# Kernel optimization log

Measured on AMD Instinct MI355X. Metric: run time of the kernel, lower is better.

The kernel has to match this reference:

```python
import jax, jax.numpy as jnp
import numpy as np

N_LAYERS = 20
EPS = 1e-7      # GENConv eps added to relu'd messages
BN_EPS = 1e-5   # torch BatchNorm1d default eps
N_NODES, N_EDGES, N_GRAPHS, D, H = 100_000, 400_000, 4096, 128, 256


def _bn(x, g, b):
    # BatchNorm1d in training mode: batch statistics over the node dim
    mu = jnp.mean(x, axis=0)
    var = jnp.var(x, axis=0)
    return (x - mu) * jax.lax.rsqrt(var + BN_EPS) * g + b


def setup_inputs() -> dict:
    key = jax.random.key(0)
    ks = jax.random.split(key, 12)
    L = N_LAYERS
    rn = lambda k, s, sc: jax.random.normal(k, s, dtype=jnp.float32) * sc
    return dict(
        x=jax.random.randint(ks[0], (N_NODES, 9), 0, 2, dtype=jnp.int32),
        edge_index=jax.random.randint(ks[1], (2, N_EDGES), 0, N_NODES, dtype=jnp.int32),
        edge_attr=jax.random.randint(ks[2], (N_EDGES, 3), 0, 2, dtype=jnp.int32),
        batch=jnp.sort(jax.random.randint(ks[3], (N_NODES,), 0, N_GRAPHS, dtype=jnp.int32)),
        # AtomEncoder: 9 tables (max size 119), padded into one array
        atom_emb=rn(ks[4], (9, 119, D), 0.1),
        # per-layer BondEncoder: 3 tables (sizes 5,6,2) padded to 6
        bond_emb=rn(ks[5], (L, 3, 6, D), 0.1),
        W1=rn(ks[6], (L, D, H), 0.05), b1=jnp.zeros((L, H), jnp.float32),
        g1=jnp.ones((L, H), jnp.float32), be1=jnp.zeros((L, H), jnp.float32),
        W2=rn(ks[7], (L, H, H), 0.05), b2=jnp.zeros((L, H), jnp.float32),
        g2=jnp.ones((L, H), jnp.float32), be2=jnp.zeros((L, H), jnp.float32),
        W3=rn(ks[8], (L, H, D), 0.05), b3=jnp.zeros((L, D), jnp.float32),
        t=jnp.ones((L,), jnp.float32),
        norm_g=jnp.ones((L, D), jnp.float32), norm_b=jnp.zeros((L, D), jnp.float32),
        predW=rn(ks[9], (D, 1), 0.05), predb=jnp.zeros((1,), jnp.float32),
    )


def _gen_conv(h, src, dst, edge_attr, bond_l, W1, b1, g1, be1, W2, b2, g2, be2, W3, b3, t):
    N = h.shape[0]
    # BondEncoder: sum of 3 embedding lookups
    eemb = bond_l[0][edge_attr[:, 0]] + bond_l[1][edge_attr[:, 1]] + bond_l[2][edge_attr[:, 2]]
    msg = jax.nn.relu(h[src] + eemb) + EPS            # [E, D]
    # scatter_softmax over destination nodes, per channel, temperature t
    scaled = msg * t
    mx = jax.ops.segment_max(scaled, dst, num_segments=N)
    mx = jnp.where(jnp.isfinite(mx), mx, 0.0)         # isolated nodes -> -inf guard
    ex = jnp.exp(scaled - mx[dst])
    denom = jax.ops.segment_sum(ex, dst, num_segments=N)
    w = ex / jnp.maximum(denom[dst], EPS)
    m = jax.ops.segment_sum(msg * w, dst, num_segments=N)
    hh = h + m
    # MLP channels [D, 2D, 2D, D], batch norm + relu on hidden layers, last linear
    a = jax.nn.relu(_bn(hh @ W1 + b1, g1, be1))
    a = jax.nn.relu(_bn(a @ W2 + b2, g2, be2))
    return a @ W3 + b3


def reference(x, edge_index, edge_attr, batch, atom_emb, bond_emb, W1, b1, g1, be1,
              W2, b2, g2, be2, W3, b3, t, norm_g, norm_b, predW, predb):
    N = x.shape[0]
    src, dst = edge_index[0], edge_index[1]
    # AtomEncoder: sum of 9 embedding lookups
    h = atom_emb[0][x[:, 0]]
    for i in range(1, 9):
        h = h + atom_emb[i][x[:, i]]
    lp = lambda l: (bond_emb[l], W1[l], b1[l], g1[l], be1[l], W2[l], b2[l],
                    g2[l], be2[l], W3[l], b3[l], t[l])
    # res+ block (dropout omitted: eval mode)
    h = _gen_conv(h, src, dst, edge_attr, *lp(0))
    for l in range(1, N_LAYERS):
        h2 = jax.nn.relu(_bn(h, norm_g[l - 1], norm_b[l - 1]))
        h = _gen_conv(h2, src, dst, edge_attr, *lp(l)) + h
    h = _bn(h, norm_g[N_LAYERS - 1], norm_b[N_LAYERS - 1])
    # global mean pool over graphs
    cnt = jax.ops.segment_sum(jnp.ones((N, 1), jnp.float32), batch, num_segments=N_GRAPHS)
    hg = jax.ops.segment_sum(h, batch, num_segments=N_GRAPHS) / jnp.maximum(cnt, 1.0)
    return hg @ predW + predb                          # [N_GRAPHS, 1]
```

## Files before the change

kernel.cpp:

```cpp
#include <hip/hip_runtime.h>
#include <math.h>

#define GEPS 1e-7f
#define BNEPS 1e-5f
#define NCOPY 32
#define CSTR 1536

typedef unsigned short u16;
typedef unsigned int   u32;

typedef _Float16 f16x8 __attribute__((ext_vector_type(8)));
typedef float    f32x4 __attribute__((ext_vector_type(4)));

__device__ __forceinline__ float h2f(u16 u){
  _Float16 x = __builtin_bit_cast(_Float16, u); return (float)x;
}
__device__ __forceinline__ u16 f2h(float f){
  _Float16 x = (_Float16)f; return __builtin_bit_cast(u16, x);
}

typedef __attribute__((address_space(1))) const void* as1p;
typedef __attribute__((address_space(3))) void*       as3p;
__device__ __forceinline__ void dma16(const u16* g, _Float16* l){
  __builtin_amdgcn_global_load_lds((as1p)g, (as3p)l, 16, 0, 0);
}

__global__ __launch_bounds__(256) void k_zero_i(int* __restrict__ p, int n){
  int i = blockIdx.x*256 + threadIdx.x;
  if (i < n) p[i] = 0;
}
__global__ __launch_bounds__(256) void k_zero_f(float* __restrict__ p, int n){
  int i = blockIdx.x*256 + threadIdx.x;
  if (i < n) p[i] = 0.f;
}

__global__ __launch_bounds__(256) void k_hist(const int* __restrict__ dst, int E,
                                              int* __restrict__ cnt){
  int e = blockIdx.x*256 + threadIdx.x;
  if (e < E) atomicAdd(&cnt[dst[e]], 1);
}

__global__ __launch_bounds__(256) void k_blocksum(const int* __restrict__ cnt, int N,
                                                  int* __restrict__ part){
  __shared__ int s[256];
  int t = threadIdx.x, i = blockIdx.x*256 + t;
  s[t] = (i < N) ? cnt[i] : 0;
  __syncthreads();
  for (int off = 128; off > 0; off >>= 1){
    if (t < off) s[t] += s[t + off];
    __syncthreads();
  }
  if (t == 0) part[blockIdx.x] = s[0];
}

__global__ __launch_bounds__(1024) void k_scanpart(int* __restrict__ part, int NB){
  __shared__ int s[1024];
  int t = threadIdx.x;
  int v = (t < NB) ? part[t] : 0;
  s[t] = v;
  __syncthreads();
  for (int off = 1; off < 1024; off <<= 1){
    int u = (t >= off) ? s[t-off] : 0;
    __syncthreads();
    s[t] += u;
    __syncthreads();
  }
  if (t < NB) part[t] = s[t] - v;
}

__global__ __launch_bounds__(256) void k_scanapply(const int* __restrict__ cnt,
    const int* __restrict__ part, int N, int E,
    int* __restrict__ offs, int* __restrict__ cursor){
  __shared__ int s[256];
  int t = threadIdx.x, i = blockIdx.x*256 + t;
  int v = (i < N) ? cnt[i] : 0;
  s[t] = v;
  __syncthreads();
  for (int off = 1; off < 256; off <<= 1){
    int u = (t >= off) ? s[t-off] : 0;
    __syncthreads();
    s[t] += u;
    __syncthreads();
  }
  int ex = part[blockIdx.x] + s[t] - v;
  if (i < N){
    offs[i]   = ex;
    cursor[i] = ex;
    if (i == N-1) offs[N] = ex + v;
  }
}

__global__ __launch_bounds__(256) void k_scatter(const int* __restrict__ src,
    const int* __restrict__ dst, const int* __restrict__ attr, int E,
    int* __restrict__ cursor, int* __restrict__ esort){
  int e = blockIdx.x*256 + threadIdx.x;
  if (e >= E) return;
  int d = dst[e];
  int pos = atomicAdd(&cursor[d], 1);
  int a = (src[e] & 0x1ffff)
        | ((attr[3*(size_t)e]   & 15) << 17)
        | ((attr[3*(size_t)e+1] & 15) << 21)
        | ((attr[3*(size_t)e+2] & 15) << 25);
  esort[pos] = a;
}

__global__ __launch_bounds__(256) void k_wtrans(const float* __restrict__ W,
    u16* __restrict__ Wt, int K, int Nout, int total){
  int id = blockIdx.x*256 + threadIdx.x;
  if (id >= total) return;
  int k   = id % K;
  int rem = id / K;
  int n   = rem % Nout;
  int l   = rem / Nout;
  Wt[id] = f2h(W[((size_t)l*K + k)*Nout + n]);
}

__global__ __launch_bounds__(256) void k_atom(const int* __restrict__ x,
    const float* __restrict__ emb, float* __restrict__ h, u16* __restrict__ h16, int N){
  int d = threadIdx.x & 127;
  int n = (blockIdx.x << 1) + (threadIdx.x >> 7);
  if (n >= N) return;
  float s = 0.f;
  #pragma unroll
  for (int i = 0; i < 9; ++i){
    int idx = x[(size_t)n*9 + i];
    s += emb[((size_t)i*119 + idx)*128 + d];
  }
  h[(size_t)n*128 + d]   = s;
  h16[(size_t)n*128 + d] = f2h(s);
}

__global__ __launch_bounds__(256) void k_redstats(const float* __restrict__ Cl,
                                                  float* __restrict__ out){
  int t = threadIdx.x;
  float s = 0.f;
  #pragma unroll
  for (int c = 0; c < NCOPY; ++c) s += Cl[c*CSTR + 1024 + t];
  out[t] = s;
}

template<bool PRE_BN>
__global__ __launch_bounds__(256)
void k_edge(const u16* __restrict__ h16,
    const int* __restrict__ offs, const int* __restrict__ esort,
    const float* __restrict__ bond,
    const float* __restrict__ tptr,
    const float* __restrict__ ssum_, const float* __restrict__ ssq_,
    const float* __restrict__ g, const float* __restrict__ b,
    u16* __restrict__ hh, int N, float invN){
  __shared__ float sg[128], sv[128];
  int tid = threadIdx.x;
  if (PRE_BN){
    if (tid < 128){
      float mu  = ssum_[tid]*invN;
      float var = fmaxf(ssq_[tid]*invN - mu*mu, 0.f);
      float rs  = rsqrtf(var + BNEPS);
      float s   = g[tid]*rs;
      sg[tid] = s;
      sv[tid] = b[tid] - mu*s;
    }
    __syncthreads();
  }
  int lane = tid & 63;
  int n = (blockIdx.x << 2) + (tid >> 6);
  if (n >= N) return;
  int c0 = lane << 1;
  float tl = *tptr;
  float sg0=1.f, sv0=0.f, sg1=1.f, sv1=0.f;
  if (PRE_BN){ sg0=sg[c0]; sv0=sv[c0]; sg1=sg[c0+1]; sv1=sv[c0+1]; }

  int s0 = offs[n], s1 = offs[n+1];
  float den0 = 0.f, acc0 = 0.f, den1 = 0.f, acc1 = 0.f;
  if (s0 < s1){
    int se = esort[s0];
    int sidx = se & 0x1ffff;
    u32 hv = *(const u32*)(h16 + (size_t)sidx*128 + c0);
    float2 e0 = *(const float2*)(bond + ((se>>17)&15)*128 + c0);
    float2 e1 = *(const float2*)(bond + (6 + ((se>>21)&15))*128 + c0);
    float2 e2 = *(const float2*)(bond + (12 + ((se>>25)&15))*128 + c0);
    for (int e = s0; e < s1; ++e){
      u32 hvN = hv; float2 e0N = e0, e1N = e1, e2N = e2;
      if (e + 1 < s1){
        int seN = esort[e+1];
        int sidxN = seN & 0x1ffff;
        hvN = *(const u32*)(h16 + (size_t)sidxN*128 + c0);
        e0N = *(const float2*)(bond + ((seN>>17)&15)*128 + c0);
        e1N = *(const float2*)(bond + (6 + ((seN>>21)&15))*128 + c0);
        e2N = *(const float2*)(bond + (12 + ((seN>>25)&15))*128 + c0);
      }
      float x0 = h2f((u16)(hv & 0xffff));
      float x1 = h2f((u16)(hv >> 16));
      if (PRE_BN){
        x0 = fmaxf(x0*sg0 + sv0, 0.f);
        x1 = fmaxf(x1*sg1 + sv1, 0.f);
      }
      float m0 = fmaxf(x0 + e0.x + e1.x + e2.x, 0.f) + GEPS;
      float m1 = fmaxf(x1 + e0.y + e1.y + e2.y, 0.f) + GEPS;
      float p0 = __expf(m0*tl);
      float p1 = __expf(m1*tl);
      den0 += p0; acc0 += p0*m0;
      den1 += p1; acc1 += p1*m1;
      hv = hvN; e0 = e0N; e1 = e1N; e2 = e2N;
    }
  }
  u32 hv = *(const u32*)(h16 + (size_t)n*128 + c0);
  float x0 = h2f((u16)(hv & 0xffff));
  float x1 = h2f((u16)(hv >> 16));
  if (PRE_BN){
    x0 = fmaxf(x0*sg0 + sv0, 0.f);
    x1 = fmaxf(x1*sg1 + sv1, 0.f);
  }
  float r0 = x0 + acc0 / fmaxf(den0, GEPS);
  float r1 = x1 + acc1 / fmaxf(den1, GEPS);
  u32 pk = (u32)f2h(r0) | ((u32)f2h(r1) << 16);
  *((u32*)hh + (size_t)n*64 + lane) = pk;
}

template<bool TRANSFORM, bool OUT32>
__global__ __launch_bounds__(256)
void k_gemm(const u16* __restrict__ A, int lda,
            const u16* __restrict__ Wt,
            const float* __restrict__ bias,
            const float* __restrict__ sIn, const float* __restrict__ qIn,
            const float* __restrict__ gam, const float* __restrict__ bet,
            const float* __restrict__ resid,
            void* __restrict__ outv, int ldo,
            u16* __restrict__ out16,
            float* __restrict__ sOut, float* __restrict__ qOut,
            int M, int K){
  __shared__ __align__(16) _Float16 As[2][4096];
  __shared__ __align__(16) _Float16 Bs[2][4096];
  __shared__ float sc[256], shv[256];
  __shared__ float redS[256], redQ[256];

  int tid = threadIdx.x;
  int lane = tid & 63;
  int w    = tid >> 6;
  int wm = w & 1, wn = w >> 1;
  int quad = lane >> 4, ln = lane & 15;
  int mBase = blockIdx.x * 128;
  int cBase = blockIdx.y * 128;

  int dc0 = tid, dc1 = 256 + tid;
  int f0 = dc0 >> 6, l20 = dc0 & 63;
  int f1 = dc1 >> 6, l21 = dc1 & 63;
  int kA0 = (l20 >> 4) << 3, kA1 = (l21 >> 4) << 3;
  int rA0 = mBase + f0*16 + (l20 & 15); if (rA0 >= M) rA0 = M - 1;
  int rA1 = mBase + f1*16 + (l21 & 15); if (rA1 >= M) rA1 = M - 1;
  const u16* apA0 = A + (size_t)rA0*lda + kA0;
  const u16* apA1 = A + (size_t)rA1*lda + kA1;
  const u16* bp0  = Wt + (size_t)(cBase + f0*16 + (l20 & 15))*K + kA0;
  const u16* bp1  = Wt + (size_t)(cBase + f1*16 + (l21 & 15))*K + kA1;

  dma16(apA0, &As[0][dc0*8]);
  dma16(apA1, &As[0][dc1*8]);
  dma16(bp0,  &Bs[0][dc0*8]);
  dma16(bp1,  &Bs[0][dc1*8]);

  if (TRANSFORM){
    float inv = 1.f/(float)M;
    for (int k = tid; k < K; k += 256){
      float s_ = 0.f, q_ = 0.f;
      #pragma unroll
      for (int c = 0; c < NCOPY; ++c){ s_ += sIn[c*CSTR + k]; q_ += qIn[c*CSTR + k]; }
      float mu  = s_*inv;
      float var = fmaxf(q_*inv - mu*mu, 0.f);
      float rs  = rsqrtf(var + BNEPS);
      float sg  = gam[k]*rs;
      sc[k]  = sg;
      shv[k] = bet[k] - mu*sg;
    }
  }

  f32x4 acc[4][4];
  #pragma unroll
  for (int i = 0; i < 4; ++i)
    #pragma unroll
    for (int j = 0; j < 4; ++j)
      acc[i][j] = (f32x4){0.f,0.f,0.f,0.f};

  int kTiles = K >> 5;
  for (int kt = 0; kt < kTiles; ++kt){
    __syncthreads();
    int cb = kt & 1, nbuf = cb ^ 1;
    if (kt + 1 < kTiles){
      int k1 = (kt + 1) << 5;
      dma16(apA0 + k1, &As[nbuf][dc0*8]);
      dma16(apA1 + k1, &As[nbuf][dc1*8]);
      dma16(bp0 + k1,  &Bs[nbuf][dc0*8]);
      dma16(bp1 + k1,  &Bs[nbuf][dc1*8]);
    }
    f16x8 af[4], bf[4];
    #pragma unroll
    for (int i = 0; i < 4; ++i)
      af[i] = *(const f16x8*)(&As[cb][(4*wm + i)*512 + lane*8]);
    if (TRANSFORM){
      int kb = kt*32 + quad*8;
      f32x4 s0 = *(const f32x4*)(&sc[kb]);
      f32x4 s1 = *(const f32x4*)(&sc[kb+4]);
      f32x4 v0 = *(const f32x4*)(&shv[kb]);
      f32x4 v1 = *(const f32x4*)(&shv[kb+4]);
      #pragma unroll
      for (int i = 0; i < 4; ++i){
        f16x8 a = af[i], o;
        o[0] = (_Float16)fmaxf((float)a[0]*s0[0] + v0[0], 0.f);
        o[1] = (_Float16)fmaxf((float)a[1]*s0[1] + v0[1], 0.f);
        o[2] = (_Float16)fmaxf((float)a[2]*s0[2] + v0[2], 0.f);
        o[3] = (_Float16)fmaxf((float)a[3]*s0[3] + v0[3], 0.f);
        o[4] = (_Float16)fmaxf((float)a[4]*s1[0] + v1[0], 0.f);
        o[5] = (_Float16)fmaxf((float)a[5]*s1[1] + v1[1], 0.f);
        o[6] = (_Float16)fmaxf((float)a[6]*s1[2] + v1[2], 0.f);
        o[7] = (_Float16)fmaxf((float)a[7]*s1[3] + v1[3], 0.f);
        af[i] = o;
      }
    }
    #pragma unroll
    for (int j = 0; j < 4; ++j)
      bf[j] = *(const f16x8*)(&Bs[cb][(4*wn + j)*512 + lane*8]);
    #pragma unroll
    for (int i = 0; i < 4; ++i)
      #pragma unroll
      for (int j = 0; j < 4; ++j)
        acc[i][j] = __builtin_amdgcn_mfma_f32_16x16x32_f16(af[i], bf[j], acc[i][j], 0, 0, 0);
  }

  float bv[4];
  #pragma unroll
  for (int j = 0; j < 4; ++j) bv[j] = bias[cBase + 64*wn + 16*j + ln];
  float ps[4] = {0,0,0,0}, pq[4] = {0,0,0,0};

  #pragma unroll
  for (int i = 0; i < 4; ++i){
    int rbase = mBase + 64*wm + 16*i + quad*4;
    #pragma unroll
    for (int r = 0; r < 4; ++r){
      int row = rbase + r;
      if (row < M){
        #pragma unroll
        for (int j = 0; j < 4; ++j){
          int col = cBase + 64*wn + 16*j + ln;
          size_t off = (size_t)row*ldo + col;
          float v = acc[i][j][r] + bv[j];
          if (OUT32){
            float* out = (float*)outv;
            if (resid) v += resid[off];
            out[off] = v;
            if (out16) out16[off] = f2h(v);
            ps[j] += v; pq[j] += v*v;
          } else {
            u16* out = (u16*)outv;
            u16 q = f2h(v);
            out[off] = q;
            float vr = h2f(q);
            ps[j] += vr; pq[j] += vr*vr;
          }
        }
      }
    }
  }
  #pragma unroll
  for (int j = 0; j < 4; ++j){
    float s = ps[j], q = pq[j];
    s += __shfl_xor(s, 16, 64);  q += __shfl_xor(q, 16, 64);
    s += __shfl_xor(s, 32, 64);  q += __shfl_xor(q, 32, 64);
    if (quad == 0){
      int col = 64*wn + 16*j + ln;
      redS[wm*128 + col] = s;
      redQ[wm*128 + col] = q;
    }
  }
  __syncthreads();
  if (tid < 128){
    float s = redS[tid] + redS[128 + tid];
    float q = redQ[tid] + redQ[128 + tid];
    int cof = (blockIdx.x & (NCOPY-1))*CSTR + cBase + tid;
    atomicAdd(&sOut[cof], s);
    atomicAdd(&qOut[cof], q);
  }
}

__global__ __launch_bounds__(256) void k_pool(const float* __restrict__ h,
    const float* __restrict__ ssum, const float* __restrict__ ssq,
    const float* __restrict__ g, const float* __restrict__ b,
    const float* __restrict__ predW, const int* __restrict__ batch,
    float* __restrict__ pool, float* __restrict__ cnt, int N){
  int lane = threadIdx.x & 63;
  int n = (blockIdx.x << 2) + (threadIdx.x >> 6);
  if (n >= N) return;
  float inv = 1.f / (float)N;
  float v = 0.f;
  #pragma unroll
  for (int d = lane; d < 128; d += 64){
    float mu  = ssum[d]*inv;
    float var = fmaxf(ssq[d]*inv - mu*mu, 0.f);
    float rs  = rsqrtf(var + BNEPS);
    float bn  = (h[(size_t)n*128 + d] - mu)*(g[d]*rs) + b[d];
    v += bn * predW[d];
  }
  #pragma unroll
  for (int off = 32; off > 0; off >>= 1) v += __shfl_down(v, off, 64);
  if (lane == 0){
    int gi = batch[n];
    atomicAdd(&pool[gi], v);
    atomicAdd(&cnt[gi], 1.f);
  }
}

__global__ __launch_bounds__(256) void k_final(const float* __restrict__ pool,
    const float* __restrict__ cnt, const float* __restrict__ predb,
    float* __restrict__ out, int G){
  int g = blockIdx.x*256 + threadIdx.x;
  if (g < G) out[g] = pool[g] / fmaxf(cnt[g], 1.f) + predb[0];
}

extern "C" void kernel_launch(void* const* d_in, const int* in_sizes, int n_in,
                              void* d_out, int out_size, void* d_ws, size_t ws_size,
                              hipStream_t stream){
  const int*   x        = (const int*)d_in[0];
  const int*   eidx     = (const int*)d_in[1];
  const int*   eattr    = (const int*)d_in[2];
  const int*   batch    = (const int*)d_in[3];
  const float* atom_emb = (const float*)d_in[4];
  const float* bond_emb = (const float*)d_in[5];
  const float* W1 = (const float*)d_in[6];
  const float* b1 = (const float*)d_in[7];
  const float* g1 = (const float*)d_in[8];
  const float* be1= (const float*)d_in[9];
  const float* W2 = (const float*)d_in[10];
  const float* b2 = (const float*)d_in[11];
  const float* g2 = (const float*)d_in[12];
  const float* be2= (const float*)d_in[13];
  const float* W3 = (const float*)d_in[14];
  const float* b3 = (const float*)d_in[15];
  const float* tt = (const float*)d_in[16];
  const float* ng = (const float*)d_in[17];
  const float* nb = (const float*)d_in[18];
  const float* predW = (const float*)d_in[19];
  const float* predb = (const float*)d_in[20];
  float* out = (float*)d_out;

  const int N = in_sizes[3];
  const int E = in_sizes[1] / 2;
  const int L = in_sizes[16];
  const int G = out_size;
  const int D = 128, H = 256;
  const float invN = 1.f / (float)N;

  char* ws = (char*)d_ws;
  size_t off = 0;
  auto carve = [&](size_t bytes)->void*{
    void* p = ws + off;
    off += (bytes + 511) & ~(size_t)511;
    return p;
  };
  float* h   = (float*)carve((size_t)N*D*4);
  u16*   y1  = (u16*)  carve((size_t)N*H*2);
  u16*   y2  = (u16*)  carve((size_t)N*H*2);
  u16*   hh  = y2;
  u16*   h16 = y1;
  u16*   Wt1 = (u16*) carve((size_t)L*H*D*2);
  u16*   Wt2 = (u16*) carve((size_t)L*H*H*2);
  u16*   Wt3 = (u16*) carve((size_t)L*D*H*2);
  int*  offs   = (int*)carve((size_t)(N+1)*4);
  int*  cursor = (int*)carve((size_t)N*4);
  int*  cnt    = (int*)carve((size_t)N*4);
  int*  part   = (int*)carve(1024*4);
  int*  esort  = (int*)carve((size_t)E*4);
  float* stats = (float*)carve((size_t)L*NCOPY*CSTR*4);
  float* fstat = (float*)carve((size_t)L*256*4);
  float* pool = (float*)carve((size_t)G*4);
  float* cntg = (float*)carve((size_t)G*4);

  int NB = (N + 255) / 256;

  k_zero_i   <<<NB, 256, 0, stream>>>(cnt, N);
  k_hist     <<<(E+255)/256, 256, 0, stream>>>(eidx + E, E, cnt);
  k_blocksum <<<NB, 256, 0, stream>>>(cnt, N, part);
  k_scanpart <<<1, 1024, 0, stream>>>(part, NB);
  k_scanapply<<<NB, 256, 0, stream>>>(cnt, part, N, E, offs, cursor);
  k_scatter  <<<(E+255)/256, 256, 0, stream>>>(eidx, eidx + E, eattr, E, cursor, esort);
  k_atom     <<<(N+1)/2, 256, 0, stream>>>(x, atom_emb, h, h16, N);
  k_zero_f   <<<(L*NCOPY*CSTR+255)/256, 256, 0, stream>>>(stats, L*NCOPY*CSTR);

  k_wtrans<<<((L*H*D)+255)/256, 256, 0, stream>>>(W1, Wt1, D, H, L*H*D);
  k_wtrans<<<((L*H*H)+255)/256, 256, 0, stream>>>(W2, Wt2, H, H, L*H*H);
  k_wtrans<<<((L*D*H)+255)/256, 256, 0, stream>>>(W3, Wt3, H, D, L*D*H);

  int mb = (N + 127) / 128;
  int eb = (N + 3) / 4;
  for (int l = 0; l < L; ++l){
    float* Cl = stats + (size_t)l*NCOPY*CSTR;
    const float* bondl = bond_emb + (size_t)l*3*6*D;
    if (l == 0){
      k_edge<false><<<eb, 256, 0, stream>>>(h16, offs, esort, bondl, tt + l,
          nullptr, nullptr, nullptr, nullptr, hh, N, invN);
    } else {
      float* fs = fstat + (size_t)(l-1)*256;
      k_edge<true><<<eb, 256, 0, stream>>>(h16, offs, esort, bondl, tt + l,
          fs, fs + 128, ng + (size_t)(l-1)*D, nb + (size_t)(l-1)*D,
          hh, N, invN);
    }
    k_gemm<false,false><<<dim3(mb,2), 256, 0, stream>>>(hh, D,
        Wt1 + (size_t)l*H*D, b1 + (size_t)l*H,
        nullptr, nullptr, nullptr, nullptr, nullptr,
        y1, H, nullptr, Cl + 0, Cl + 256, N, D);
    k_gemm<true,false><<<dim3(mb,2), 256, 0, stream>>>(y1, H,
        Wt2 + (size_t)l*H*H, b2 + (size_t)l*H,
        Cl + 0, Cl + 256, g1 + (size_t)l*H, be1 + (size_t)l*H, nullptr,
        y2, H, nullptr, Cl + 512, Cl + 768, N, H);
    k_gemm<true,true><<<dim3(mb,1), 256, 0, stream>>>(y2, H,
        Wt3 + (size_t)l*D*H, b3 + (size_t)l*D,
        Cl + 512, Cl + 768, g2 + (size_t)l*H, be2 + (size_t)l*H,
        (l ? h : nullptr),
        h, D, h16, Cl + 1024, Cl + 1152, N, H);
    k_redstats<<<1, 256, 0, stream>>>(Cl, fstat + (size_t)l*256);
  }

  float* fsL = fstat + (size_t)(L-1)*256;
  k_zero_f<<<(G+255)/256, 256, 0, stream>>>(pool, G);
  k_zero_f<<<(G+255)/256, 256, 0, stream>>>(cntg, G);
  k_pool  <<<(N+3)/4, 256, 0, stream>>>(h, fsL, fsL + 128,
      ng + (size_t)(L-1)*D, nb + (size_t)(L-1)*D, predW, batch, pool, cntg, N);
  k_final <<<(G+255)/256, 256, 0, stream>>>(pool, cntg, predb, out, G);
}
```

Baseline: 4.860 ms.

## Precombine bond embeddings and shrink GEMM M-tile to 64 rows

Precomputes, per layer, all 72 combinations of the three bond embedding tables, so the edge kernel does one float2 lookup per edge instead of three loads and two adds. Separately, the GEMM block tile shrinks from 128 to 64 rows, with each of the four waves covering all 64 rows and 32 columns. This doubles the grid and removes the LDS cross-wave stats reduction and its barrier, at the cost of more global atomics on the stats copies and less reuse of the B tile per block.

```diff
diff --git a/kernel.cpp b/kernel.cpp
--- a/kernel.cpp
+++ b/kernel.cpp
@@ -97,11 +97,20 @@
   if (e >= E) return;
   int d = dst[e];
   int pos = atomicAdd(&cursor[d], 1);
-  int a = (src[e] & 0x1ffff)
-        | ((attr[3*(size_t)e]   & 15) << 17)
-        | ((attr[3*(size_t)e+1] & 15) << 21)
-        | ((attr[3*(size_t)e+2] & 15) << 25);
-  esort[pos] = a;
+  int comb = attr[3*(size_t)e]*12 + attr[3*(size_t)e+1]*2 + attr[3*(size_t)e+2];
+  esort[pos] = (src[e] & 0x1ffff) | (comb << 17);
+}
+
+__global__ __launch_bounds__(256) void k_comb(const float* __restrict__ bond_emb,
+    float* __restrict__ comb, int total){
+  int id = blockIdx.x*256 + threadIdx.x;
+  if (id >= total) return;
+  int d = id & 127;
+  int c = (id >> 7) % 72;
+  int l = (id >> 7) / 72;
+  int a0 = c/12, a1 = (c/2)%6, a2 = c&1;
+  const float* b = bond_emb + (size_t)l*3*6*128;
+  comb[id] = b[a0*128 + d] + b[(6 + a1)*128 + d] + b[(12 + a2)*128 + d];
 }
 
 __global__ __launch_bounds__(256) void k_wtrans(const float* __restrict__ W,
@@ -143,7 +152,7 @@
 __global__ __launch_bounds__(256)
 void k_edge(const u16* __restrict__ h16,
     const int* __restrict__ offs, const int* __restrict__ esort,
-    const float* __restrict__ bond,
+    const float* __restrict__ comb,
     const float* __restrict__ tptr,
     const float* __restrict__ ssum_, const float* __restrict__ ssq_,
     const float* __restrict__ g, const float* __restrict__ b,
@@ -173,20 +182,14 @@
   float den0 = 0.f, acc0 = 0.f, den1 = 0.f, acc1 = 0.f;
   if (s0 < s1){
     int se = esort[s0];
-    int sidx = se & 0x1ffff;
-    u32 hv = *(const u32*)(h16 + (size_t)sidx*128 + c0);
-    float2 e0 = *(const float2*)(bond + ((se>>17)&15)*128 + c0);
-    float2 e1 = *(const float2*)(bond + (6 + ((se>>21)&15))*128 + c0);
-    float2 e2 = *(const float2*)(bond + (12 + ((se>>25)&15))*128 + c0);
+    u32 hv = *(const u32*)(h16 + (size_t)(se & 0x1ffff)*128 + c0);
+    float2 ev = *(const float2*)(comb + (se >> 17)*128 + c0);
     for (int e = s0; e < s1; ++e){
-      u32 hvN = hv; float2 e0N = e0, e1N = e1, e2N = e2;
+      u32 hvN = hv; float2 evN = ev;
       if (e + 1 < s1){
         int seN = esort[e+1];
-        int sidxN = seN & 0x1ffff;
-        hvN = *(const u32*)(h16 + (size_t)sidxN*128 + c0);
-        e0N = *(const float2*)(bond + ((seN>>17)&15)*128 + c0);
-        e1N = *(const float2*)(bond + (6 + ((seN>>21)&15))*128 + c0);
-        e2N = *(const float2*)(bond + (12 + ((seN>>25)&15))*128 + c0);
+        hvN = *(const u32*)(h16 + (size_t)(seN & 0x1ffff)*128 + c0);
+        evN = *(const float2*)(comb + (seN >> 17)*128 + c0);
       }
       float x0 = h2f((u16)(hv & 0xffff));
       float x1 = h2f((u16)(hv >> 16));
@@ -194,13 +197,13 @@
         x0 = fmaxf(x0*sg0 + sv0, 0.f);
         x1 = fmaxf(x1*sg1 + sv1, 0.f);
       }
-      float m0 = fmaxf(x0 + e0.x + e1.x + e2.x, 0.f) + GEPS;
-      float m1 = fmaxf(x1 + e0.y + e1.y + e2.y, 0.f) + GEPS;
+      float m0 = fmaxf(x0 + ev.x, 0.f) + GEPS;
+      float m1 = fmaxf(x1 + ev.y, 0.f) + GEPS;
       float p0 = __expf(m0*tl);
       float p1 = __expf(m1*tl);
       den0 += p0; acc0 += p0*m0;
       den1 += p1; acc1 += p1*m1;
-      hv = hvN; e0 = e0N; e1 = e1N; e2 = e2N;
+      hv = hvN; ev = evN;
     }
   }
   u32 hv = *(const u32*)(h16 + (size_t)n*128 + c0);
@@ -228,34 +231,31 @@
             u16* __restrict__ out16,
             float* __restrict__ sOut, float* __restrict__ qOut,
             int M, int K){
-  __shared__ __align__(16) _Float16 As[2][4096];
+  __shared__ __align__(16) _Float16 As[2][2048];
   __shared__ __align__(16) _Float16 Bs[2][4096];
   __shared__ float sc[256], shv[256];
-  __shared__ float redS[256], redQ[256];
 
   int tid = threadIdx.x;
   int lane = tid & 63;
-  int w    = tid >> 6;
-  int wm = w & 1, wn = w >> 1;
+  int wn   = tid >> 6;
   int quad = lane >> 4, ln = lane & 15;
-  int mBase = blockIdx.x * 128;
+  int mBase = blockIdx.x * 64;
   int cBase = blockIdx.y * 128;
 
+  int fA = tid >> 6, lA = tid & 63;
+  int kA = (lA >> 4) << 3;
+  int rA = mBase + fA*16 + (lA & 15); if (rA >= M) rA = M - 1;
+  const u16* apA = A + (size_t)rA*lda + kA;
   int dc0 = tid, dc1 = 256 + tid;
   int f0 = dc0 >> 6, l20 = dc0 & 63;
   int f1 = dc1 >> 6, l21 = dc1 & 63;
-  int kA0 = (l20 >> 4) << 3, kA1 = (l21 >> 4) << 3;
-  int rA0 = mBase + f0*16 + (l20 & 15); if (rA0 >= M) rA0 = M - 1;
-  int rA1 = mBase + f1*16 + (l21 & 15); if (rA1 >= M) rA1 = M - 1;
-  const u16* apA0 = A + (size_t)rA0*lda + kA0;
-  const u16* apA1 = A + (size_t)rA1*lda + kA1;
-  const u16* bp0  = Wt + (size_t)(cBase + f0*16 + (l20 & 15))*K + kA0;
-  const u16* bp1  = Wt + (size_t)(cBase + f1*16 + (l21 & 15))*K + kA1;
-
-  dma16(apA0, &As[0][dc0*8]);
-  dma16(apA1, &As[0][dc1*8]);
-  dma16(bp0,  &Bs[0][dc0*8]);
-  dma16(bp1,  &Bs[0][dc1*8]);
+  int kB0 = (l20 >> 4) << 3, kB1 = (l21 >> 4) << 3;
+  const u16* bp0 = Wt + (size_t)(cBase + f0*16 + (l20 & 15))*K + kB0;
+  const u16* bp1 = Wt + (size_t)(cBase + f1*16 + (l21 & 15))*K + kB1;
+
+  dma16(apA, &As[0][dc0*8]);
+  dma16(bp0, &Bs[0][dc0*8]);
+  dma16(bp1, &Bs[0][dc1*8]);
 
   if (TRANSFORM){
     float inv = 1.f/(float)M;
@@ -272,11 +272,11 @@
     }
   }
 
-  f32x4 acc[4][4];
+  f32x4 acc[4][2];
   #pragma unroll
   for (int i = 0; i < 4; ++i)
     #pragma unroll
-    for (int j = 0; j < 4; ++j)
+    for (int j = 0; j < 2; ++j)
       acc[i][j] = (f32x4){0.f,0.f,0.f,0.f};
 
   int kTiles = K >> 5;
@@ -285,15 +285,14 @@
     int cb = kt & 1, nbuf = cb ^ 1;
     if (kt + 1 < kTiles){
       int k1 = (kt + 1) << 5;
-      dma16(apA0 + k1, &As[nbuf][dc0*8]);
-      dma16(apA1 + k1, &As[nbuf][dc1*8]);
-      dma16(bp0 + k1,  &Bs[nbuf][dc0*8]);
-      dma16(bp1 + k1,  &Bs[nbuf][dc1*8]);
-    }
-    f16x8 af[4], bf[4];
+      dma16(apA + k1, &As[nbuf][dc0*8]);
+      dma16(bp0 + k1, &Bs[nbuf][dc0*8]);
+      dma16(bp1 + k1, &Bs[nbuf][dc1*8]);
+    }
+    f16x8 af[4], bf[2];
     #pragma unroll
     for (int i = 0; i < 4; ++i)
-      af[i] = *(const f16x8*)(&As[cb][(4*wm + i)*512 + lane*8]);
+      af[i] = *(const f16x8*)(&As[cb][i*512 + lane*8]);
     if (TRANSFORM){
       int kb = kt*32 + quad*8;
       f32x4 s0 = *(const f32x4*)(&sc[kb]);
@@ -315,42 +314,41 @@
       }
     }
     #pragma unroll
-    for (int j = 0; j < 4; ++j)
-      bf[j] = *(const f16x8*)(&Bs[cb][(4*wn + j)*512 + lane*8]);
+    for (int j = 0; j < 2; ++j)
+      bf[j] = *(const f16x8*)(&Bs[cb][(2*wn + j)*512 + lane*8]);
     #pragma unroll
     for (int i = 0; i < 4; ++i)
       #pragma unroll
-      for (int j = 0; j < 4; ++j)
+      for (int j = 0; j < 2; ++j)
         acc[i][j] = __builtin_amdgcn_mfma_f32_16x16x32_f16(af[i], bf[j], acc[i][j], 0, 0, 0);
   }
 
-  float bv[4];
-  #pragma unroll
-  for (int j = 0; j < 4; ++j) bv[j] = bias[cBase + 64*wn + 16*j + ln];
-  float ps[4] = {0,0,0,0}, pq[4] = {0,0,0,0};
+  float bv[2];
+  #pragma unroll
+  for (int j = 0; j < 2; ++j) bv[j] = bias[cBase + (2*wn + j)*16 + ln];
+  float ps[2] = {0,0}, pq[2] = {0,0};
 
   #pragma unroll
   for (int i = 0; i < 4; ++i){
-    int rbase = mBase + 64*wm + 16*i + quad*4;
     #pragma unroll
     for (int r = 0; r < 4; ++r){
-      int row = rbase + r;
+      int row = mBase + 16*i + quad*4 + r;
       if (row < M){
+        size_t base = (size_t)row*ldo;
         #pragma unroll
-        for (int j = 0; j < 4; ++j){
-          int col = cBase + 64*wn + 16*j + ln;
-          size_t off = (size_t)row*ldo + col;
+        for (int j = 0; j < 2; ++j){
+          int col = cBase + (2*wn + j)*16 + ln;
           float v = acc[i][j][r] + bv[j];
           if (OUT32){
             float* out = (float*)outv;
-            if (resid) v += resid[off];
-            out[off] = v;
-            if (out16) out16[off] = f2h(v);
+            if (resid) v += resid[base + col];
+            out[base + col] = v;
+            if (out16) out16[base + col] = f2h(v);
             ps[j] += v; pq[j] += v*v;
           } else {
             u16* out = (u16*)outv;
             u16 q = f2h(v);
-            out[off] = q;
+            out[base + col] = q;
             float vr = h2f(q);
             ps[j] += vr; pq[j] += vr*vr;
           }
@@ -359,23 +357,15 @@
     }
   }
   #pragma unroll
-  for (int j = 0; j < 4; ++j){
+  for (int j = 0; j < 2; ++j){
     float s = ps[j], q = pq[j];
     s += __shfl_xor(s, 16, 64);  q += __shfl_xor(q, 16, 64);
     s += __shfl_xor(s, 32, 64);  q += __shfl_xor(q, 32, 64);
     if (quad == 0){
-      int col = 64*wn + 16*j + ln;
-      redS[wm*128 + col] = s;
-      redQ[wm*128 + col] = q;
-    }
-  }
-  __syncthreads();
-  if (tid < 128){
-    float s = redS[tid] + redS[128 + tid];
-    float q = redQ[tid] + redQ[128 + tid];
-    int cof = (blockIdx.x & (NCOPY-1))*CSTR + cBase + tid;
-    atomicAdd(&sOut[cof], s);
-    atomicAdd(&qOut[cof], q);
+      int cof = (blockIdx.x & (NCOPY-1))*CSTR + cBase + (2*wn + j)*16 + ln;
+      atomicAdd(&sOut[cof], s);
+      atomicAdd(&qOut[cof], q);
+    }
   }
 }
 
@@ -466,6 +456,7 @@
   int*  cnt    = (int*)carve((size_t)N*4);
   int*  part   = (int*)carve(1024*4);
   int*  esort  = (int*)carve((size_t)E*4);
+  float* comb  = (float*)carve((size_t)L*72*128*4);
   float* stats = (float*)carve((size_t)L*NCOPY*CSTR*4);
   float* fstat = (float*)carve((size_t)L*256*4);
   float* pool = (float*)carve((size_t)G*4);
@@ -481,22 +472,23 @@
   k_scatter  <<<(E+255)/256, 256, 0, stream>>>(eidx, eidx + E, eattr, E, cursor, esort);
   k_atom     <<<(N+1)/2, 256, 0, stream>>>(x, atom_emb, h, h16, N);
   k_zero_f   <<<(L*NCOPY*CSTR+255)/256, 256, 0, stream>>>(stats, L*NCOPY*CSTR);
+  k_comb     <<<((L*72*128)+255)/256, 256, 0, stream>>>(bond_emb, comb, L*72*128);
 
   k_wtrans<<<((L*H*D)+255)/256, 256, 0, stream>>>(W1, Wt1, D, H, L*H*D);
   k_wtrans<<<((L*H*H)+255)/256, 256, 0, stream>>>(W2, Wt2, H, H, L*H*H);
   k_wtrans<<<((L*D*H)+255)/256, 256, 0, stream>>>(W3, Wt3, H, D, L*D*H);
 
-  int mb = (N + 127) / 128;
+  int mb = (N + 63) / 64;
   int eb = (N + 3) / 4;
   for (int l = 0; l < L; ++l){
     float* Cl = stats + (size_t)l*NCOPY*CSTR;
-    const float* bondl = bond_emb + (size_t)l*3*6*D;
+    const float* combl = comb + (size_t)l*72*128;
     if (l == 0){
-      k_edge<false><<<eb, 256, 0, stream>>>(h16, offs, esort, bondl, tt + l,
+      k_edge<false><<<eb, 256, 0, stream>>>(h16, offs, esort, combl, tt + l,
           nullptr, nullptr, nullptr, nullptr, hh, N, invN);
     } else {
       float* fs = fstat + (size_t)(l-1)*256;
-      k_edge<true><<<eb, 256, 0, stream>>>(h16, offs, esort, bondl, tt + l,
+      k_edge<true><<<eb, 256, 0, stream>>>(h16, offs, esort, combl, tt + l,
           fs, fs + 128, ng + (size_t)(l-1)*D, nb + (size_t)(l-1)*D,
           hh, N, invN);
     }
```

Result: slower. 4.958 ms (+2.0%).
